# Kernel optimization log

Hardware: AMD Instinct MI355X
Metric: run time of the kernel (lower is better)

## Reference

```python
import jax, jax.numpy as jnp
import numpy as np
import math

B, T, C = 2, 1024, 1024
H = 16
HS = C // H          # head size 64
ROT = HS // 2        # rotary dims 32
TT = 1024            # ctx_len
FFN = 4 * C
EPS = 1e-6


def _layernorm(x, g, b):
    m = jnp.mean(x, -1, keepdims=True)
    v = jnp.mean((x - m) ** 2, -1, keepdims=True)
    return (x - m) * jax.lax.rsqrt(v + EPS) * g + b


def _time_shift_half(x):
    # ZeroPad2d((0,0,1,-1)) applied to first half of channels: shift by one step in time
    c = x.shape[-1]
    a = jnp.pad(x[:, :, : c // 2], ((0, 0), (1, 0), (0, 0)))[:, :-1, :]
    return jnp.concatenate([a, x[:, :, c // 2 :]], axis=-1)


def _rotate_half(x):
    x1, x2 = jnp.split(x, 2, axis=-1)
    return jnp.concatenate([-x2, x1], axis=-1)


def _rotary_cos_sin(t_len, rot, base):
    inv_freq = 1.0 / (base ** (jnp.arange(0, rot, 2, dtype=jnp.float32) / rot))
    freqs = jnp.arange(t_len, dtype=jnp.float32)[:, None] * inv_freq[None, :]
    emb = jnp.concatenate([freqs, freqs], axis=-1)  # (T, rot)
    return jnp.cos(emb), jnp.sin(emb)


def _build_w(time_w, time_alpha, time_beta, t_len):
    # faithful translation of the pad/tile/reshape circulant trick
    w = jnp.pad(time_w, ((0, 0), (0, TT)))            # (H, 2TT)
    w = jnp.tile(w, (1, TT))                          # (H, 2TT*TT)
    w = w[:, :-TT].reshape(-1, TT, 2 * TT - 1)        # (H, TT, 2TT-1)
    w = w[:, :, TT - 1 :]                             # (H, TT, TT)
    return w[:, :t_len, :t_len] * time_alpha[:, :, :t_len] * time_beta[:, :t_len, :]


def setup_inputs() -> dict:
    key = jax.random.key(0)
    ks = jax.random.split(key, 24)
    s = 0.02
    d = {
        "x": jax.random.normal(ks[0], (B, T, C), jnp.float32),
        "ln1_g": jnp.ones((C,), jnp.float32),
        "ln1_b": jnp.zeros((C,), jnp.float32),
        "Wq": jax.random.normal(ks[1], (C, C), jnp.float32) * s,
        "bq": jnp.zeros((C,), jnp.float32),
        "Wk": jax.random.normal(ks[2], (C, C), jnp.float32) * s,
        "bk": jnp.zeros((C,), jnp.float32),
        "Wv": jax.random.normal(ks[3], (C, C), jnp.float32) * s,
        "bv": jnp.zeros((C,), jnp.float32),
        "Wo": jax.random.normal(ks[4], (C, C), jnp.float32) * s,
        "bo": jnp.zeros((C,), jnp.float32),
        "time_w": 1.0 + 0.01 * jax.random.normal(ks[5], (H, TT), jnp.float32),
        "time_alpha": 1.0 + 0.01 * jax.random.normal(ks[6], (H, 1, TT), jnp.float32),
        "time_beta": 1.0 + 0.01 * jax.random.normal(ks[7], (H, TT, 1), jnp.float32),
        "time_gamma": 1.0 + 0.01 * jax.random.normal(ks[8], (TT, 1), jnp.float32),
        "Wmix": jnp.eye(H, dtype=jnp.float32) + 0.01 * jax.random.normal(ks[9], (H, H), jnp.float32),
        "ln2_g": jnp.ones((C,), jnp.float32),
        "ln2_b": jnp.zeros((C,), jnp.float32),
        "Wgk": jax.random.normal(ks[10], (C, FFN), jnp.float32) * s,
        "bgk": jnp.zeros((FFN,), jnp.float32),
        "Wgv": jax.random.normal(ks[11], (C, FFN), jnp.float32) * s,
        "bgv": jnp.zeros((FFN,), jnp.float32),
        "Wgw": jax.random.normal(ks[12], (FFN, C), jnp.float32) * s,
        "bgw": jnp.zeros((C,), jnp.float32),
    }
    return d


def _block(x, ln1_g, ln1_b, Wq, bq, Wk, bk, Wv, bv, Wo, bo,
           time_w, time_alpha, time_beta, time_gamma, Wmix,
           ln2_g, ln2_b, Wgk, bgk, Wgv, bgv, Wgw, bgw):
    b, t, c = x.shape
    # ---- MHA_pro attention sublayer (pre-LN residual) ----
    xs = _time_shift_half(_layernorm(x, ln1_g, ln1_b))
    q = (xs @ Wq + bq).reshape(b, t, H, HS).transpose(0, 2, 1, 3)  # bhtd
    k = (xs @ Wk + bk).reshape(b, t, H, HS).transpose(0, 2, 1, 3)
    v = (xs @ Wv + bv).reshape(b, t, H, HS).transpose(0, 2, 1, 3)
    qr, qp = q[..., :ROT], q[..., ROT:]
    kr, kp = k[..., :ROT], k[..., ROT:]
    cos, sin = _rotary_cos_sin(t, ROT, float(TT))  # base = ctx_len
    qr = qr * cos + _rotate_half(qr) * sin
    kr = kr * cos + _rotate_half(kr) * sin
    q = jnp.concatenate([qr, qp], axis=-1)
    k = jnp.concatenate([kr, kp], axis=-1)
    att = jnp.einsum("bhtd,bhud->bhtu", q, k) * (1.0 / math.sqrt(HS))
    causal = jnp.tril(jnp.ones((t, t), bool))
    att = jnp.where(causal, att, -jnp.inf)
    att = jax.nn.softmax(att, axis=-1)
    w = _build_w(time_w, time_alpha, time_beta, t)  # (H, T, T)
    att = att * w[None]
    att = jnp.einsum("ij,bjtu->bitu", Wmix, att)  # 1x1 conv head mix
    y = jnp.einsum("bhtu,bhud->bhtd", att, v)
    y = y.transpose(0, 2, 1, 3).reshape(b, t, c)
    y = (y @ Wo + bo) * time_gamma[:t, :]
    x = x + y
    # ---- GeGLU MLP sublayer (pre-LN residual) ----
    xm = _layernorm(x, ln2_g, ln2_b)
    kk = xm @ Wgk + bgk
    vv = xm @ Wgv + bgv
    y2 = (jax.nn.gelu(kk, approximate=False) * vv) @ Wgw + bgw
    return x + y2


def reference(x, ln1_g, ln1_b, Wq, bq, Wk, bk, Wv, bv, Wo, bo,
              time_w, time_alpha, time_beta, time_gamma, Wmix,
              ln2_g, ln2_b, Wgk, bgk, Wgv, bgv, Wgw, bgw):
    return _block(x, ln1_g, ln1_b, Wq, bq, Wk, bk, Wv, bv, Wo, bo,
                  time_w, time_alpha, time_beta, time_gamma, Wmix,
                  ln2_g, ln2_b, Wgk, bgk, Wgv, bgv, Wgw, bgw)
```

## Files before the change

kernel.cpp:

```cpp
#include <hip/hip_runtime.h>
#include <math.h>

typedef unsigned short u16;
typedef short s16x8 __attribute__((ext_vector_type(8)));
typedef float f32x4 __attribute__((ext_vector_type(4)));

#define TB 2
#define TSEQ 1024
#define CC 1024
#define NH 16
#define HSZ 64
#define FFN 4096
#define MROWS (TB*TSEQ)

#define GLOAD16(g, l) __builtin_amdgcn_global_load_lds( \
    (const __attribute__((address_space(1))) unsigned*)(g), \
    (__attribute__((address_space(3))) unsigned*)(l), 16, 0, 0)

#define SBAR()  __builtin_amdgcn_s_barrier()
#define SCHED0() __builtin_amdgcn_sched_barrier(0)
#define LGKM0() asm volatile("s_waitcnt lgkmcnt(0)" ::: "memory")
#define WAITV4() asm volatile("s_waitcnt vmcnt(4)" ::: "memory")
#define PRIO(n) __builtin_amdgcn_s_setprio(n)

__device__ __forceinline__ float bf2f(u16 u){
  union { unsigned u; float f; } c; c.u = ((unsigned)u) << 16; return c.f;
}
__device__ __forceinline__ u16 f2bf(float f){
  union { float f; unsigned u; } c; c.f = f;
  unsigned u = c.u;
  u += 0x7fffu + ((u >> 16) & 1);
  return (u16)(u >> 16);
}
__device__ __forceinline__ float ldin(const void* p, size_t i, int bf){
  return bf ? bf2f(((const u16*)p)[i]) : ((const float*)p)[i];
}

__global__ void k_flag(const unsigned* __restrict__ g, int* __restrict__ flag){
  if (threadIdx.x == 0) *flag = (g[0] == 0x3F800000u) ? 0 : 1;
}

__global__ void k_transpose_cvt(const void* __restrict__ in, u16* __restrict__ out,
                                int R, int Cc, const int* __restrict__ flagp){
  int bf = *flagp;
  __shared__ u16 tile[32][33];
  int bx = blockIdx.x * 32, by = blockIdx.y * 32;
  int tx = threadIdx.x & 31, ty = threadIdx.x >> 5;
  #pragma unroll
  for (int i = 0; i < 32; i += 8)
    tile[ty + i][tx] = f2bf(ldin(in, (size_t)(by + ty + i) * Cc + bx + tx, bf));
  __syncthreads();
  #pragma unroll
  for (int i = 0; i < 32; i += 8)
    out[(size_t)(bx + ty + i) * R + by + tx] = tile[tx][ty + i];
}

__global__ void k_cvt(const void* __restrict__ in, u16* __restrict__ out, int n,
                      const int* __restrict__ flagp){
  int bf = *flagp;
  int i = blockIdx.x * 256 + threadIdx.x;
  if (i < n) out[i] = f2bf(ldin(in, i, bf));
}

__global__ void k_tw8(const void* __restrict__ tw, u16* __restrict__ tw8,
                      const int* __restrict__ flagp){
  int bf = *flagp;
  int idx = blockIdx.x*256 + threadIdx.x;
  int s = idx >> 14;
  int h = (idx >> 10) & 15;
  int k = idx & 1023;
  float v = (k + s < 1024) ? ldin(tw, h*1024 + k + s, bf) : 0.f;
  tw8[idx] = f2bf(v);
}

__global__ void k_ln1_shift(const void* __restrict__ x, const void* __restrict__ g,
                            const void* __restrict__ bta, u16* __restrict__ xs,
                            const int* __restrict__ flagp){
  int bf = *flagp;
  int row = blockIdx.x;
  int t = row & (TSEQ - 1);
  int tid = threadIdx.x;
  float v[4]; float s = 0.f, ss = 0.f;
  #pragma unroll
  for (int i = 0; i < 4; i++){
    v[i] = ldin(x, (size_t)row * CC + tid*4 + i, bf);
    s += v[i]; ss += v[i]*v[i];
  }
  __shared__ float rs[256], rss[256];
  rs[tid] = s; rss[tid] = ss; __syncthreads();
  for (int o = 128; o > 0; o >>= 1){ if (tid < o){ rs[tid] += rs[tid+o]; rss[tid] += rss[tid+o]; } __syncthreads(); }
  float mean = rs[0] * (1.0f/CC);
  float var  = rss[0] * (1.0f/CC) - mean*mean;
  float inv  = rsqrtf(var + 1e-6f);
  #pragma unroll
  for (int i = 0; i < 4; i++){
    int c = tid*4 + i;
    float o = (v[i]-mean)*inv*ldin(g, c, bf) + ldin(bta, c, bf);
    u16 ob = f2bf(o);
    if (c >= CC/2)            xs[(size_t)row*CC + c] = ob;
    else if (t < TSEQ-1)      xs[(size_t)(row+1)*CC + c] = ob;
  }
  if (t == 0 && tid < 128){
    #pragma unroll
    for (int i = 0; i < 4; i++) xs[(size_t)row*CC + tid*4 + i] = 0;
  }
}

__global__ void k_ln2(const float* __restrict__ x1, const void* __restrict__ g,
                      const void* __restrict__ bta, u16* __restrict__ xm,
                      const int* __restrict__ flagp){
  int bf = *flagp;
  int row = blockIdx.x;
  int tid = threadIdx.x;
  const float* xr = x1 + (size_t)row * CC;
  float v[4]; float s = 0.f, ss = 0.f;
  #pragma unroll
  for (int i = 0; i < 4; i++){ v[i] = xr[tid*4 + i]; s += v[i]; ss += v[i]*v[i]; }
  __shared__ float rs[256], rss[256];
  rs[tid] = s; rss[tid] = ss; __syncthreads();
  for (int o = 128; o > 0; o >>= 1){ if (tid < o){ rs[tid] += rs[tid+o]; rss[tid] += rss[tid+o]; } __syncthreads(); }
  float mean = rs[0] * (1.0f/CC);
  float var  = rss[0] * (1.0f/CC) - mean*mean;
  float inv  = rsqrtf(var + 1e-6f);
  #pragma unroll
  for (int i = 0; i < 4; i++){
    int c = tid*4 + i;
    xm[(size_t)row*CC + c] = f2bf((v[i]-mean)*inv*ldin(g, c, bf) + ldin(bta, c, bf));
  }
}

__global__ void k_rotary(u16* __restrict__ qkv){
  int idx = blockIdx.x*256 + threadIdx.x;
  int i = idx & 15;
  int h = (idx >> 4) & (NH-1);
  int row = idx >> 8;
  int t = row & (TSEQ-1);
  float invf = exp2f(-0.625f * (float)i);
  float ang = (float)t * invf;
  float cs = cosf(ang), sn = sinf(ang);
  size_t base = (size_t)row * (3*CC);
  u16* qp = qkv + base + h*HSZ;
  float a = bf2f(qp[i]), b2 = bf2f(qp[i+16]);
  qp[i]    = f2bf(a*cs - b2*sn);
  qp[i+16] = f2bf(b2*cs + a*sn);
  u16* kp = qkv + base + CC + h*HSZ;
  a = bf2f(kp[i]); b2 = bf2f(kp[i+16]);
  kp[i]    = f2bf(a*cs - b2*sn);
  kp[i+16] = f2bf(b2*cs + a*sn);
}

__global__ __launch_bounds__(256) void k_qk(
    const u16* __restrict__ qkv, u16* __restrict__ att)
{
  int m0 = blockIdx.y * 128;
  int n0 = blockIdx.x * 128;
  if (n0 > m0) return;
  int bh = blockIdx.z; int b = bh >> 4, h = bh & 15;
  __shared__ u16 As[128*32];
  __shared__ u16 Bs[128*32];
  int tid = threadIdx.x;
  int w = tid >> 6;
  int lane = tid & 63;
  int wm = (w >> 1) * 64, wn = (w & 1) * 64;
  f32x4 acc[4][4];
  #pragma unroll
  for (int i = 0; i < 4; i++)
    #pragma unroll
    for (int j = 0; j < 4; j++) acc[i][j] = (f32x4){0.f,0.f,0.f,0.f};

  int rr = lane >> 2;
  int cc = lane & 3;
  const u16* gA0 = qkv + (size_t)(b*TSEQ + m0 + w*32 + rr)*(3*CC) + h*HSZ + cc*8;
  const u16* gA1 = gA0 + (size_t)16*(3*CC);
  const u16* gB0 = qkv + (size_t)(b*TSEQ + n0 + w*32 + rr)*(3*CC) + CC + h*HSZ + cc*8;
  const u16* gB1 = gB0 + (size_t)16*(3*CC);
  u16* lA0 = As + (w*32)*32;
  u16* lA1 = As + (w*32+16)*32;
  u16* lB0 = Bs + (w*32)*32;
  u16* lB1 = Bs + (w*32+16)*32;
  int quad = lane >> 4;
  int l15 = lane & 15;

  #pragma unroll
  for (int k0 = 0; k0 < HSZ; k0 += 32){
    __syncthreads();
    GLOAD16(gA0 + k0, lA0);
    GLOAD16(gA1 + k0, lA1);
    GLOAD16(gB0 + k0, lB0);
    GLOAD16(gB1 + k0, lB1);
    __syncthreads();
    s16x8 af[4], bfr[4];
    #pragma unroll
    for (int i = 0; i < 4; i++){
      af[i]  = *(s16x8*)&As[(wm + i*16 + l15)*32 + quad*8];
      bfr[i] = *(s16x8*)&Bs[(wn + i*16 + l15)*32 + quad*8];
    }
    #pragma unroll
    for (int mi = 0; mi < 4; mi++)
      #pragma unroll
      for (int ni = 0; ni < 4; ni++)
        acc[mi][ni] = __builtin_amdgcn_mfma_f32_16x16x32_bf16(af[mi], bfr[ni], acc[mi][ni], 0, 0, 0);
  }

  #pragma unroll
  for (int mi = 0; mi < 4; mi++){
    int rowb = m0 + wm + mi*16 + quad*4;
    #pragma unroll
    for (int ni = 0; ni < 4; ni++){
      int col = n0 + wn + ni*16 + l15;
      #pragma unroll
      for (int r = 0; r < 4; r++){
        int t = rowb + r;
        att[((size_t)bh*TSEQ + t)*TSEQ + col] = f2bf(acc[mi][ni][r] * 0.125f);
      }
    }
  }
}

__global__ __launch_bounds__(256) void k_softmix(
    u16* __restrict__ att, const u16* __restrict__ tw8, const u16* __restrict__ al16,
    const u16* __restrict__ be16, const void* __restrict__ wmix,
    const int* __restrict__ flagp)
{
  int bf = *flagp;
  int bt = blockIdx.x;
  int t = bt & (TSEQ-1);
  int b = bt >> 10;
  int tid = threadIdx.x;
  int wv = tid >> 6;
  int lane = tid & 63;
  int tile_end = ((t >> 7) + 1) << 7;
  int nchunk = (t >> 9) + 1;
  int sh = (TSEQ-1 - t) & 7;
  int base = (TSEQ-1 - t) - sh;
  __shared__ __align__(16) u16 P[NH][TSEQ];
  __shared__ float wm[NH*NH];
  if (tid < NH*NH) wm[tid] = ldin(wmix, tid, bf);

  #pragma unroll
  for (int hi = 0; hi < 4; hi++){
    int h = wv*4 + hi;
    const u16* srow = att + ((size_t)(b*NH + h)*TSEQ + t)*TSEQ;
    const u16* twp  = tw8 + ((size_t)sh*NH + h)*TSEQ + base;
    const u16* alp  = al16 + h*TSEQ;
    float v[16];
    float lmax = -1e30f;
    for (int r = 0; r < nchunk; r++){
      int ub = lane*8 + r*512;
      uint4 pk = *(const uint4*)(srow + ub);
      const u16* pe = (const u16*)&pk;
      #pragma unroll
      for (int e = 0; e < 8; e++){
        float s = bf2f(pe[e]);
        if (ub + e > t) s = -1e30f;
        v[r*8+e] = s;
        lmax = fmaxf(lmax, s);
      }
    }
    #pragma unroll
    for (int o = 32; o > 0; o >>= 1) lmax = fmaxf(lmax, __shfl_xor(lmax, o));
    float lsum = 0.f;
    for (int r = 0; r < nchunk; r++){
      #pragma unroll
      for (int e = 0; e < 8; e++){
        float p = __expf(v[r*8+e] - lmax);
        v[r*8+e] = p; lsum += p;
      }
    }
    #pragma unroll
    for (int o = 32; o > 0; o >>= 1) lsum += __shfl_xor(lsum, o);
    float btv = bf2f(be16[h*TSEQ + t]);
    float inv = btv / lsum;
    for (int r = 0; r < nchunk; r++){
      int ub = lane*8 + r*512;
      uint4 wk = *(const uint4*)(twp + ub);
      uint4 ak = *(const uint4*)(alp + ub);
      const u16* we = (const u16*)&wk;
      const u16* ae = (const u16*)&ak;
      u16 tmp[8];
      #pragma unroll
      for (int e = 0; e < 8; e++){
        float p = v[r*8+e] * inv * bf2f(we[e]) * bf2f(ae[e]);
        tmp[e] = f2bf(p);
      }
      *(uint4*)&P[h][ub] = *(uint4*)tmp;
    }
  }
  __syncthreads();

  int u0 = tid * 4;
  if (u0 < tile_end){
    #pragma unroll
    for (int half2 = 0; half2 < 2; half2++){
      float acc[8][4];
      #pragma unroll
      for (int i = 0; i < 8; i++)
        #pragma unroll
        for (int k = 0; k < 4; k++) acc[i][k] = 0.f;
      #pragma unroll
      for (int j = 0; j < 16; j++){
        uint2 pk = *(const uint2*)&P[j][u0];
        float p0 = bf2f((u16)(pk.x & 0xffff)), p1 = bf2f((u16)(pk.x >> 16));
        float p2 = bf2f((u16)(pk.y & 0xffff)), p3 = bf2f((u16)(pk.y >> 16));
        #pragma unroll
        for (int i2 = 0; i2 < 8; i2++){
          float w = wm[(half2*8 + i2)*NH + j];
          acc[i2][0] += w*p0; acc[i2][1] += w*p1; acc[i2][2] += w*p2; acc[i2][3] += w*p3;
        }
      }
      #pragma unroll
      for (int i2 = 0; i2 < 8; i2++){
        int i = half2*8 + i2;
        u16 tmp[4] = {f2bf(acc[i2][0]), f2bf(acc[i2][1]), f2bf(acc[i2][2]), f2bf(acc[i2][3])};
        *(uint2*)(att + ((size_t)(b*NH + i)*TSEQ + t)*TSEQ + u0) = *(uint2*)tmp;
      }
    }
  }
}

__global__ void k_vt(const u16* __restrict__ qkv, u16* __restrict__ vt){
  __shared__ u16 tile[32][33];
  int bh = blockIdx.z; int b = bh >> 4, h = bh & 15;
  int u0 = blockIdx.x * 32, d0 = blockIdx.y * 32;
  int tx = threadIdx.x & 31, ty = threadIdx.x >> 5;
  #pragma unroll
  for (int i = 0; i < 32; i += 8)
    tile[ty + i][tx] = qkv[(size_t)(b*TSEQ + u0 + ty + i)*(3*CC) + 2*CC + h*HSZ + d0 + tx];
  __syncthreads();
  #pragma unroll
  for (int i = 0; i < 32; i += 8)
    vt[((size_t)bh*HSZ + d0 + ty + i)*TSEQ + u0 + tx] = tile[tx][ty + i];
}

__global__ void k_gelumul(const u16* __restrict__ kkvv, u16* __restrict__ hh){
  int idx = blockIdx.x*256 + threadIdx.x;
  int m = idx >> 9;
  int j = (idx & 511) * 8;
  uint4 kk4 = *(const uint4*)(kkvv + (size_t)m*(2*FFN) + j);
  uint4 vv4 = *(const uint4*)(kkvv + (size_t)m*(2*FFN) + FFN + j);
  const u16* ks = (const u16*)&kk4;
  const u16* vs = (const u16*)&vv4;
  u16 out[8];
  #pragma unroll
  for (int e = 0; e < 8; e++){
    float kk = bf2f(ks[e]), vv = bf2f(vs[e]);
    float ge = 0.5f*kk*(1.0f + erff(kk*0.70710678f));
    out[e] = f2bf(ge*vv);
  }
  *(uint4*)(hh + (size_t)m*FFN + j) = *(uint4*)out;
}

__global__ __launch_bounds__(512, 2) void k_gemm256(
    const u16* __restrict__ A, const u16* __restrict__ Bt,
    const u16* __restrict__ bias, int M, int N, int K, int mode,
    u16* __restrict__ outp, float* __restrict__ partial)
{
  __shared__ u16 S[65536];
  u16* SA0 = S;
  u16* SB0 = S + 16384;
  u16* SA1 = S + 32768;
  u16* SB1 = S + 49152;

  int nwg = (int)(gridDim.x * gridDim.y * gridDim.z);
  int lin = (int)(blockIdx.x + gridDim.x * (blockIdx.y + gridDim.y * blockIdx.z));
  int nl  = (nwg & 7) ? lin : ((lin & 7) * (nwg >> 3) + (lin >> 3));
  int bx  = nl % (int)gridDim.x;
  int tq  = nl / (int)gridDim.x;
  int by  = tq % (int)gridDim.y;
  int bz  = tq / (int)gridDim.y;

  int m0 = by * 256, n0 = bx * 256;
  int kper = K / (int)gridDim.z;
  int kbeg = bz * kper;
  int nt = kper >> 6;
  int niter = nt >> 1;

  int tid = threadIdx.x;
  int w = tid >> 6, lane = tid & 63;
  int wm = w >> 2, wn = w & 3;
  int quad = lane >> 4, l15 = lane & 15;
  int l3 = lane >> 3, ch = (lane & 7) ^ l3;

  const u16* gA = A  + (size_t)(m0 + w*16 + l3) * K + ch*8 + kbeg;
  const u16* gB = Bt + (size_t)(n0 + w*16 + l3) * K + ch*8 + kbeg;
  const size_t hstep = (size_t)128 * K;
  const size_t rstep = (size_t)8 * K;

  int pc0 = quad ^ (l15 & 7);
  int pc1 = (4 + quad) ^ (l15 & 7);
  int aoff0 = (wm*128 + l15)*64 + pc0*8;
  int aoff1 = (wm*128 + l15)*64 + pc1*8;
  int boff0 = (wn*64 + l15)*64 + pc0*8;
  int boff1 = (wn*64 + l15)*64 + pc1*8;

  f32x4 acc[8][4];
  #pragma unroll
  for (int i = 0; i < 8; i++)
    #pragma unroll
    for (int j = 0; j < 4; j++) acc[i][j] = (f32x4){0.f,0.f,0.f,0.f};

  #define STG(gbase, sbase, h, ko) do{ \
      const u16* _g = (gbase) + (size_t)(h)*hstep + (ko); \
      u16* _l = (sbase) + ((h)*128 + w*16)*64; \
      GLOAD16(_g, _l); \
      GLOAD16(_g + rstep, _l + 512); \
    }while(0)

  #define LD_A(buf, MQ) do{ _Pragma("unroll") for (int _m = 0; _m < 4; _m++){ \
      a0[_m] = *(const s16x8*)((buf) + aoff0 + (MQ)*4096 + _m*1024); \
      a1[_m] = *(const s16x8*)((buf) + aoff1 + (MQ)*4096 + _m*1024); } }while(0)

  #define LD_B(buf, NQ, B0A, B1A) do{ _Pragma("unroll") for (int _n = 0; _n < 2; _n++){ \
      B0A[_n] = *(const s16x8*)((buf) + boff0 + (NQ)*2048 + _n*1024); \
      B1A[_n] = *(const s16x8*)((buf) + boff1 + (NQ)*2048 + _n*1024); } }while(0)

  #define MMQ(MQ, NQ, B0A, B1A) do{ _Pragma("unroll") for (int _m = 0; _m < 4; _m++){ \
      _Pragma("unroll") for (int _n = 0; _n < 2; _n++){ \
        acc[(MQ)*4+_m][(NQ)*2+_n] = __builtin_amdgcn_mfma_f32_16x16x32_bf16(a0[_m], B0A[_n], acc[(MQ)*4+_m][(NQ)*2+_n], 0, 0, 0); \
        acc[(MQ)*4+_m][(NQ)*2+_n] = __builtin_amdgcn_mfma_f32_16x16x32_bf16(a1[_m], B1A[_n], acc[(MQ)*4+_m][(NQ)*2+_n], 0, 0, 0); }} }while(0)

  STG(gB, SB0, 0, 0); STG(gB, SB0, 1, 0);
  STG(gA, SA0, 0, 0); STG(gA, SA0, 1, 0);
  STG(gB, SB1, 0, 64); STG(gB, SB1, 1, 64);
  WAITV4();
  SBAR();

  s16x8 a0[4], a1[4], bl0[2], bl1[2], bh0[2], bh1[2];

  for (int i = 0; i < niter; i++){
    int t1k = (2*i+1)*64;
    int t2k = (2*i+2 < nt) ? (2*i+2)*64 : 0;
    int t3k = (2*i+3 < nt) ? (2*i+3)*64 : 0;

    LD_A(SA0, 0); LD_B(SB0, 0, bl0, bl1);
    STG(gA, SA1, 0, t1k);
    SBAR(); LGKM0(); SCHED0(); PRIO(1); MMQ(0,0,bl0,bl1); PRIO(0); SBAR();
    LD_B(SB0, 1, bh0, bh1);
    STG(gA, SA1, 1, t1k);
    SBAR(); LGKM0(); SCHED0(); PRIO(1); MMQ(0,1,bh0,bh1); PRIO(0); SBAR();
    LD_A(SA0, 1);
    STG(gB, SB0, 0, t2k);
    SBAR(); LGKM0(); SCHED0(); PRIO(1); MMQ(1,0,bl0,bl1); PRIO(0); SBAR();
    STG(gB, SB0, 1, t2k);
    SBAR(); LGKM0(); SCHED0(); PRIO(1); MMQ(1,1,bh0,bh1); PRIO(0);
    WAITV4(); SBAR();
    LD_A(SA1, 0); LD_B(SB1, 0, bl0, bl1);
    STG(gA, SA0, 0, t2k);
    SBAR(); LGKM0(); SCHED0(); PRIO(1); MMQ(0,0,bl0,bl1); PRIO(0); SBAR();
    LD_B(SB1, 1, bh0, bh1);
    STG(gA, SA0, 1, t2k);
    SBAR(); LGKM0(); SCHED0(); PRIO(1); MMQ(0,1,bh0,bh1); PRIO(0); SBAR();
    LD_A(SA1, 1);
    STG(gB, SB1, 0, t3k);
    SBAR(); LGKM0(); SCHED0(); PRIO(1); MMQ(1,0,bl0,bl1); PRIO(0); SBAR();
    STG(gB, SB1, 1, t3k);
    SBAR(); LGKM0(); SCHED0(); PRIO(1); MMQ(1,1,bh0,bh1); PRIO(0);
    WAITV4(); SBAR();
  }

  if (mode == 3){
    float* pout = partial + (size_t)bz * M * N;
    #pragma unroll
    for (int mi = 0; mi < 8; mi++){
      int rowb = m0 + wm*128 + mi*16 + quad*4;
      #pragma unroll
      for (int ni = 0; ni < 4; ni++){
        int col = n0 + wn*64 + ni*16 + l15;
        #pragma unroll
        for (int r = 0; r < 4; r++)
          pout[(size_t)(rowb + r) * N + col] = acc[mi][ni][r];
      }
    }
  } else {
    #pragma unroll
    for (int mi = 0; mi < 8; mi++){
      int rowb = m0 + wm*128 + mi*16 + quad*4;
      #pragma unroll
      for (int ni = 0; ni < 4; ni++){
        int col = n0 + wn*64 + ni*16 + l15;
        float bv = bf2f(bias[col]);
        #pragma unroll
        for (int r = 0; r < 4; r++)
          outp[(size_t)(rowb + r) * N + col] = f2bf(acc[mi][ni][r] + bv);
      }
    }
  }
  #undef STG
  #undef LD_A
  #undef LD_B
  #undef MMQ
}

__global__ __launch_bounds__(256) void k_gemm(
    const u16* __restrict__ A, const u16* __restrict__ Bt,
    const u16* __restrict__ bias, int M, int N, int K, int mode,
    void* __restrict__ outp, const void* __restrict__ xres,
    const float* __restrict__ resf, const u16* __restrict__ gamma,
    float* __restrict__ partial, const int* __restrict__ flagp)
{
  int bf = *flagp;
  __shared__ u16 As[128*32];
  __shared__ u16 Bs[128*32];
  int tid = threadIdx.x;
  int m0 = blockIdx.y * 128;
  int n0 = blockIdx.x * 128;
  int nz = gridDim.z;
  int kper = K / nz;
  int kbeg = blockIdx.z * kper;
  int kend = kbeg + kper;
  int w = tid >> 6;
  int lane = tid & 63;
  int wm = (w >> 1) * 64, wn = (w & 1) * 64;
  f32x4 acc[4][4];
  #pragma unroll
  for (int i = 0; i < 4; i++)
    #pragma unroll
    for (int j = 0; j < 4; j++) acc[i][j] = (f32x4){0.f,0.f,0.f,0.f};

  int rr = lane >> 2;
  int cc = lane & 3;
  const u16* gA0 = A  + (size_t)(m0 + w*32 + rr)*K + cc*8;
  const u16* gA1 = gA0 + (size_t)16*K;
  const u16* gB0 = Bt + (size_t)(n0 + w*32 + rr)*K + cc*8;
  const u16* gB1 = gB0 + (size_t)16*K;
  u16* lA0 = As + (w*32)*32;
  u16* lA1 = As + (w*32+16)*32;
  u16* lB0 = Bs + (w*32)*32;
  u16* lB1 = Bs + (w*32+16)*32;
  int quad = lane >> 4;
  int l15 = lane & 15;

  for (int k0 = kbeg; k0 < kend; k0 += 32){
    __syncthreads();
    GLOAD16(gA0 + k0, lA0);
    GLOAD16(gA1 + k0, lA1);
    GLOAD16(gB0 + k0, lB0);
    GLOAD16(gB1 + k0, lB1);
    __syncthreads();
    s16x8 af[4], bfr[4];
    #pragma unroll
    for (int i = 0; i < 4; i++){
      af[i]  = *(s16x8*)&As[(wm + i*16 + l15)*32 + quad*8];
      bfr[i] = *(s16x8*)&Bs[(wn + i*16 + l15)*32 + quad*8];
    }
    #pragma unroll
    for (int mi = 0; mi < 4; mi++)
      #pragma unroll
      for (int ni = 0; ni < 4; ni++)
        acc[mi][ni] = __builtin_amdgcn_mfma_f32_16x16x32_bf16(af[mi], bfr[ni], acc[mi][ni], 0, 0, 0);
  }

  if (nz > 1){
    float* pout = partial + (size_t)blockIdx.z * M * N;
    #pragma unroll
    for (int mi = 0; mi < 4; mi++){
      int rowb = m0 + wm + mi*16 + quad*4;
      #pragma unroll
      for (int ni = 0; ni < 4; ni++){
        int col = n0 + wn + ni*16 + l15;
        #pragma unroll
        for (int r = 0; r < 4; r++)
          pout[(size_t)(rowb + r) * N + col] = acc[mi][ni][r];
      }
    }
    return;
  }

  #pragma unroll
  for (int mi = 0; mi < 4; mi++){
    int rowb = m0 + wm + mi*16 + quad*4;
    #pragma unroll
    for (int ni = 0; ni < 4; ni++){
      int col = n0 + wn + ni*16 + l15;
      float bv = bf2f(bias[col]);
      #pragma unroll
      for (int r = 0; r < 4; r++){
        int row = rowb + r;
        float val = acc[mi][ni][r] + bv;
        size_t idx = (size_t)row * N + col;
        if (mode == 0){
          ((u16*)outp)[idx] = f2bf(val);
        } else if (mode == 1){
          int t = row & (TSEQ-1);
          ((float*)outp)[idx] = ldin(xres, idx, bf) + val * bf2f(gamma[t]);
        } else {
          float o = resf[idx] + val;
          if (bf) ((u16*)outp)[idx] = f2bf(o);
          else    ((float*)outp)[idx] = o;
        }
      }
    }
  }
}

__global__ void k_reduceK(const float* __restrict__ partial, int nsplit,
                          int M, int N, const u16* __restrict__ bias, int mode,
                          void* __restrict__ outp, const void* __restrict__ xres,
                          const float* __restrict__ resf, const u16* __restrict__ gamma,
                          const int* __restrict__ flagp){
  int bf = *flagp;
  int idx = blockIdx.x*256 + threadIdx.x;
  int row = idx / (N/4);
  int c0  = (idx % (N/4)) * 4;
  size_t base = (size_t)row * N + c0;
  float v[4] = {0.f, 0.f, 0.f, 0.f};
  for (int s = 0; s < nsplit; s++){
    const float4 p = *(const float4*)(partial + (size_t)s * M * N + base);
    v[0] += p.x; v[1] += p.y; v[2] += p.z; v[3] += p.w;
  }
  #pragma unroll
  for (int e = 0; e < 4; e++) v[e] += bf2f(bias[c0 + e]);
  if (mode == 1){
    int t = row & (TSEQ-1);
    float gm = bf2f(gamma[t]);
    float o[4];
    #pragma unroll
    for (int e = 0; e < 4; e++) o[e] = ldin(xres, base + e, bf) + v[e] * gm;
    *(float4*)((float*)outp + base) = (float4){o[0], o[1], o[2], o[3]};
  } else {
    float o[4];
    #pragma unroll
    for (int e = 0; e < 4; e++) o[e] = resf[base + e] + v[e];
    if (bf){
      u16 tmp[4] = {f2bf(o[0]), f2bf(o[1]), f2bf(o[2]), f2bf(o[3])};
      *(uint2*)((u16*)outp + base) = *(uint2*)tmp;
    } else {
      *(float4*)((float*)outp + base) = (float4){o[0], o[1], o[2], o[3]};
    }
  }
}

__global__ __launch_bounds__(256) void k_pv(
    const u16* __restrict__ att, const u16* __restrict__ vt, u16* __restrict__ y)
{
  __shared__ u16 As[128*32];
  __shared__ u16 Bs[64*32];
  int tid = threadIdx.x;
  int bh = blockIdx.y; int b = bh >> 4, h = bh & 15;
  int m0 = blockIdx.x * 128;
  const u16* A  = att + (size_t)bh * TSEQ * TSEQ;
  const u16* Bt = vt  + (size_t)bh * HSZ * TSEQ;
  int w = tid >> 6;
  int lane = tid & 63;
  int wm = (w >> 1) * 64, wn = (w & 1) * 32;
  f32x4 acc[4][2];
  #pragma unroll
  for (int i = 0; i < 4; i++){ acc[i][0] = (f32x4){0,0,0,0}; acc[i][1] = (f32x4){0,0,0,0}; }

  int rr = lane >> 2;
  int cc = lane & 3;
  const u16* gA0 = A + (size_t)(m0 + w*32 + rr)*TSEQ + cc*8;
  const u16* gA1 = gA0 + (size_t)16*TSEQ;
  const u16* gB0 = Bt + (size_t)(w*16 + rr)*TSEQ + cc*8;
  u16* lA0 = As + (w*32)*32;
  u16* lA1 = As + (w*32+16)*32;
  u16* lB0 = Bs + (w*16)*32;
  int quad = lane >> 4;
  int l15 = lane & 15;
  int kend = m0 + 128;

  for (int k0 = 0; k0 < kend; k0 += 32){
    __syncthreads();
    GLOAD16(gA0 + k0, lA0);
    GLOAD16(gA1 + k0, lA1);
    GLOAD16(gB0 + k0, lB0);
    __syncthreads();
    s16x8 af[4], bfr[2];
    #pragma unroll
    for (int i = 0; i < 4; i++)
      af[i] = *(s16x8*)&As[(wm + i*16 + l15)*32 + quad*8];
    #pragma unroll
    for (int i = 0; i < 2; i++)
      bfr[i] = *(s16x8*)&Bs[(wn + i*16 + l15)*32 + quad*8];
    #pragma unroll
    for (int mi = 0; mi < 4; mi++)
      #pragma unroll
      for (int ni = 0; ni < 2; ni++)
        acc[mi][ni] = __builtin_amdgcn_mfma_f32_16x16x32_bf16(af[mi], bfr[ni], acc[mi][ni], 0, 0, 0);
  }

  #pragma unroll
  for (int mi = 0; mi < 4; mi++){
    int rowb = m0 + wm + mi*16 + quad*4;
    #pragma unroll
    for (int ni = 0; ni < 2; ni++){
      int col = wn + ni*16 + l15;
      #pragma unroll
      for (int r = 0; r < 4; r++){
        int t = rowb + r;
        y[(size_t)(b*TSEQ + t)*CC + h*HSZ + col] = f2bf(acc[mi][ni][r]);
      }
    }
  }
}

extern "C" void kernel_launch(void* const* d_in, const int* in_sizes, int n_in,
                              void* d_out, int out_size, void* d_ws, size_t ws_size,
                              hipStream_t stream){
  const void* x     = d_in[0];
  const void* ln1g  = d_in[1];
  const void* ln1b  = d_in[2];
  const void* Wq    = d_in[3];
  const void* bq    = d_in[4];
  const void* Wk    = d_in[5];
  const void* bk    = d_in[6];
  const void* Wv    = d_in[7];
  const void* bv    = d_in[8];
  const void* Wo    = d_in[9];
  const void* bo    = d_in[10];
  const void* timew = d_in[11];
  const void* alpha = d_in[12];
  const void* beta  = d_in[13];
  const void* gamma = d_in[14];
  const void* Wmix  = d_in[15];
  const void* ln2g  = d_in[16];
  const void* ln2b  = d_in[17];
  const void* Wgk   = d_in[18];
  const void* bgk   = d_in[19];
  const void* Wgv   = d_in[20];
  const void* bgv   = d_in[21];
  const void* Wgw   = d_in[22];
  const void* bgw   = d_in[23];

  char* ws = (char*)d_ws;
  size_t off = 0;
  auto carve = [&](size_t bytes)->char*{
    char* p = ws + off; off = (off + bytes + 255) & ~(size_t)255; return p;
  };
  int*  FLAG   = (int*)carve(256);
  u16*  WT_QKV = (u16*)carve(3072ull*1024*2);
  u16*  WT_O   = (u16*)carve(1024ull*1024*2);
  u16*  WT_G   = (u16*)carve(8192ull*1024*2);
  u16*  WT_W   = (u16*)carve(1024ull*4096*2);
  u16*  B_QKV  = (u16*)carve(3072*2);
  u16*  B_G    = (u16*)carve(8192*2);
  u16*  B_O    = (u16*)carve(1024*2);
  u16*  B_W    = (u16*)carve(1024*2);
  u16*  GMA    = (u16*)carve(1024*2);
  u16*  TW8    = (u16*)carve(8ull*16*1024*2 + 4096);
  u16*  AL16   = (u16*)carve(16*1024*2);
  u16*  BE16   = (u16*)carve(16*1024*2);
  u16*  XS     = (u16*)carve((size_t)MROWS*CC*2);
  u16*  QKV    = (u16*)carve((size_t)MROWS*3*CC*2);
  u16*  ATT    = (u16*)carve((size_t)TB*NH*TSEQ*TSEQ*2);
  u16*  VT     = (u16*)carve((size_t)TB*NH*HSZ*TSEQ*2);
  u16*  Y      = (u16*)carve((size_t)MROWS*CC*2);
  float* X1    = (float*)carve((size_t)MROWS*CC*4);
  u16*  XM     = (u16*)carve((size_t)MROWS*CC*2);
  u16*  KKVV   = (u16*)carve((size_t)MROWS*2*FFN*2);
  u16*  HH     = (u16*)carve((size_t)MROWS*FFN*2);
  float* PART  = (float*)ATT;
  (void)ws_size; (void)in_sizes; (void)n_in; (void)out_size;

  k_flag<<<1,64,0,stream>>>((const unsigned*)ln1g, FLAG);

  k_transpose_cvt<<<dim3(32,32),256,0,stream>>>(Wq, WT_QKV,                1024, 1024, FLAG);
  k_transpose_cvt<<<dim3(32,32),256,0,stream>>>(Wk, WT_QKV + 1024*1024,    1024, 1024, FLAG);
  k_transpose_cvt<<<dim3(32,32),256,0,stream>>>(Wv, WT_QKV + 2*1024*1024,  1024, 1024, FLAG);
  k_transpose_cvt<<<dim3(32,32),256,0,stream>>>(Wo, WT_O,                  1024, 1024, FLAG);
  k_transpose_cvt<<<dim3(128,32),256,0,stream>>>(Wgk, WT_G,                1024, 4096, FLAG);
  k_transpose_cvt<<<dim3(128,32),256,0,stream>>>(Wgv, WT_G + 4096ull*1024, 1024, 4096, FLAG);
  k_transpose_cvt<<<dim3(32,128),256,0,stream>>>(Wgw, WT_W,                4096, 1024, FLAG);
  k_cvt<<<4,256,0,stream>>>(bq, B_QKV,        1024, FLAG);
  k_cvt<<<4,256,0,stream>>>(bk, B_QKV + 1024, 1024, FLAG);
  k_cvt<<<4,256,0,stream>>>(bv, B_QKV + 2048, 1024, FLAG);
  k_cvt<<<16,256,0,stream>>>(bgk, B_G,        4096, FLAG);
  k_cvt<<<16,256,0,stream>>>(bgv, B_G + 4096, 4096, FLAG);
  k_cvt<<<4,256,0,stream>>>(bo,  B_O, 1024, FLAG);
  k_cvt<<<4,256,0,stream>>>(bgw, B_W, 1024, FLAG);
  k_cvt<<<4,256,0,stream>>>(gamma, GMA, 1024, FLAG);
  k_tw8<<<512,256,0,stream>>>(timew, TW8, FLAG);
  k_cvt<<<64,256,0,stream>>>(alpha, AL16, 16384, FLAG);
  k_cvt<<<64,256,0,stream>>>(beta,  BE16, 16384, FLAG);

  k_ln1_shift<<<MROWS,256,0,stream>>>(x, ln1g, ln1b, XS, FLAG);
  k_gemm256<<<dim3(12,8),512,0,stream>>>(XS, WT_QKV, B_QKV, MROWS, 3072, 1024, 0,
                                         QKV, nullptr);
  k_rotary<<<2048,256,0,stream>>>(QKV);
  k_qk<<<dim3(8,8,TB*NH),256,0,stream>>>(QKV, ATT);
  k_softmix<<<TB*TSEQ,256,0,stream>>>(ATT, TW8, AL16, BE16, Wmix, FLAG);
  k_vt<<<dim3(32,2,32),256,0,stream>>>(QKV, VT);
  k_pv<<<dim3(8,32),256,0,stream>>>(ATT, VT, Y);

  k_gemm<<<dim3(8,16,2),256,0,stream>>>(Y, WT_O, B_O, MROWS, 1024, 1024, 1,
                                        nullptr, nullptr, nullptr, nullptr, PART, FLAG);
  k_reduceK<<<MROWS*1024/(4*256),256,0,stream>>>(PART, 2, MROWS, 1024, B_O, 1,
                                                 X1, x, nullptr, GMA, FLAG);

  k_ln2<<<MROWS,256,0,stream>>>(X1, ln2g, ln2b, XM, FLAG);
  k_gemm256<<<dim3(32,8),512,0,stream>>>(XM, WT_G, B_G, MROWS, 8192, 1024, 0,
                                         KKVV, nullptr);
  k_gelumul<<<(MROWS*FFN)/(256*8),256,0,stream>>>(KKVV, HH);

  k_gemm256<<<dim3(4,8,8),512,0,stream>>>(HH, WT_W, nullptr, MROWS, 1024, 4096, 3,
                                          nullptr, PART);
  k_reduceK<<<MROWS*1024/(4*256),256,0,stream>>>(PART, 8, MROWS, 1024, B_W, 2,
                                                 d_out, nullptr, X1, nullptr, FLAG);
}
```

Before: 440.8 us.

## Warp-shuffle layernorm reductions, rope table, and restructured softmix loads/mixing

Replaces the shared-memory tree reductions in both layernorm kernels with wavefront shuffles plus a four-entry cross-wave sum. Precomputes the rotary cos/sin table once so the rotary kernel no longer evaluates transcendentals. In the softmax/head-mix kernel, all score rows are loaded up front together with the time-weight and alpha vectors, the chunk loops are unrolled explicitly, and the 16x16 head mix is restructured so each thread covers two columns for all heads and loops only over the causal extent. The intent is less launch, reduction and memory-latency overhead, at the cost of more registers in softmix, which now has an occupancy hint.

```diff
diff --git a/kernel.cpp b/kernel.cpp
--- a/kernel.cpp
+++ b/kernel.cpp
@@ -73,6 +73,15 @@
   tw8[idx] = f2bf(v);
 }
 
+__global__ void k_ropetab(float2* __restrict__ rt){
+  int idx = blockIdx.x*256 + threadIdx.x;
+  int i = idx & 15;
+  int t = idx >> 4;
+  float invf = exp2f(-0.625f * (float)i);
+  float ang = (float)t * invf;
+  rt[idx] = (float2){cosf(ang), sinf(ang)};
+}
+
 __global__ void k_ln1_shift(const void* __restrict__ x, const void* __restrict__ g,
                             const void* __restrict__ bta, u16* __restrict__ xs,
                             const int* __restrict__ flagp){
@@ -80,17 +89,22 @@
   int row = blockIdx.x;
   int t = row & (TSEQ - 1);
   int tid = threadIdx.x;
+  int wv = tid >> 6, lane = tid & 63;
   float v[4]; float s = 0.f, ss = 0.f;
   #pragma unroll
   for (int i = 0; i < 4; i++){
     v[i] = ldin(x, (size_t)row * CC + tid*4 + i, bf);
     s += v[i]; ss += v[i]*v[i];
   }
-  __shared__ float rs[256], rss[256];
-  rs[tid] = s; rss[tid] = ss; __syncthreads();
-  for (int o = 128; o > 0; o >>= 1){ if (tid < o){ rs[tid] += rs[tid+o]; rss[tid] += rss[tid+o]; } __syncthreads(); }
-  float mean = rs[0] * (1.0f/CC);
-  float var  = rss[0] * (1.0f/CC) - mean*mean;
+  #pragma unroll
+  for (int o = 32; o > 0; o >>= 1){ s += __shfl_xor(s, o); ss += __shfl_xor(ss, o); }
+  __shared__ float rs[4], rss[4];
+  if (lane == 0){ rs[wv] = s; rss[wv] = ss; }
+  __syncthreads();
+  float S = rs[0]+rs[1]+rs[2]+rs[3];
+  float SS = rss[0]+rss[1]+rss[2]+rss[3];
+  float mean = S * (1.0f/CC);
+  float var  = SS * (1.0f/CC) - mean*mean;
   float inv  = rsqrtf(var + 1e-6f);
   #pragma unroll
   for (int i = 0; i < 4; i++){
@@ -112,15 +126,20 @@
   int bf = *flagp;
   int row = blockIdx.x;
   int tid = threadIdx.x;
+  int wv = tid >> 6, lane = tid & 63;
   const float* xr = x1 + (size_t)row * CC;
   float v[4]; float s = 0.f, ss = 0.f;
   #pragma unroll
   for (int i = 0; i < 4; i++){ v[i] = xr[tid*4 + i]; s += v[i]; ss += v[i]*v[i]; }
-  __shared__ float rs[256], rss[256];
-  rs[tid] = s; rss[tid] = ss; __syncthreads();
-  for (int o = 128; o > 0; o >>= 1){ if (tid < o){ rs[tid] += rs[tid+o]; rss[tid] += rss[tid+o]; } __syncthreads(); }
-  float mean = rs[0] * (1.0f/CC);
-  float var  = rss[0] * (1.0f/CC) - mean*mean;
+  #pragma unroll
+  for (int o = 32; o > 0; o >>= 1){ s += __shfl_xor(s, o); ss += __shfl_xor(ss, o); }
+  __shared__ float rs[4], rss[4];
+  if (lane == 0){ rs[wv] = s; rss[wv] = ss; }
+  __syncthreads();
+  float S = rs[0]+rs[1]+rs[2]+rs[3];
+  float SS = rss[0]+rss[1]+rss[2]+rss[3];
+  float mean = S * (1.0f/CC);
+  float var  = SS * (1.0f/CC) - mean*mean;
   float inv  = rsqrtf(var + 1e-6f);
   #pragma unroll
   for (int i = 0; i < 4; i++){
@@ -129,15 +148,14 @@
   }
 }
 
-__global__ void k_rotary(u16* __restrict__ qkv){
+__global__ void k_rotary(u16* __restrict__ qkv, const float2* __restrict__ rt){
   int idx = blockIdx.x*256 + threadIdx.x;
   int i = idx & 15;
   int h = (idx >> 4) & (NH-1);
   int row = idx >> 8;
   int t = row & (TSEQ-1);
-  float invf = exp2f(-0.625f * (float)i);
-  float ang = (float)t * invf;
-  float cs = cosf(ang), sn = sinf(ang);
+  float2 cssn = rt[t*16 + i];
+  float cs = cssn.x, sn = cssn.y;
   size_t base = (size_t)row * (3*CC);
   u16* qp = qkv + base + h*HSZ;
   float a = bf2f(qp[i]), b2 = bf2f(qp[i+16]);
@@ -217,7 +235,7 @@
   }
 }
 
-__global__ __launch_bounds__(256) void k_softmix(
+__global__ __launch_bounds__(256, 4) void k_softmix(
     u16* __restrict__ att, const u16* __restrict__ tw8, const u16* __restrict__ al16,
     const u16* __restrict__ be16, const void* __restrict__ wmix,
     const int* __restrict__ flagp)
@@ -237,83 +255,98 @@
   __shared__ float wm[NH*NH];
   if (tid < NH*NH) wm[tid] = ldin(wmix, tid, bf);
 
+  uint4 raw[4][2];
+  #pragma unroll
+  for (int hi = 0; hi < 4; hi++){
+    const u16* srow = att + ((size_t)(b*NH + wv*4 + hi)*TSEQ + t)*TSEQ + lane*8;
+    raw[hi][0] = *(const uint4*)srow;
+    if (nchunk == 2) raw[hi][1] = *(const uint4*)(srow + 512);
+  }
+
   #pragma unroll
   for (int hi = 0; hi < 4; hi++){
     int h = wv*4 + hi;
-    const u16* srow = att + ((size_t)(b*NH + h)*TSEQ + t)*TSEQ;
-    const u16* twp  = tw8 + ((size_t)sh*NH + h)*TSEQ + base;
-    const u16* alp  = al16 + h*TSEQ;
-    float v[16];
+    const u16* twp = tw8 + ((size_t)sh*NH + h)*TSEQ + base + lane*8;
+    const u16* alp = al16 + h*TSEQ + lane*8;
+    uint4 wk2[2], ak2[2];
+    wk2[0] = *(const uint4*)twp;
+    ak2[0] = *(const uint4*)alp;
+    if (nchunk == 2){
+      wk2[1] = *(const uint4*)(twp + 512);
+      ak2[1] = *(const uint4*)(alp + 512);
+    }
+
+    float v0[8], v1[8];
     float lmax = -1e30f;
-    for (int r = 0; r < nchunk; r++){
-      int ub = lane*8 + r*512;
-      uint4 pk = *(const uint4*)(srow + ub);
-      const u16* pe = (const u16*)&pk;
+    {
+      const u16* pe = (const u16*)&raw[hi][0];
+      int ub = lane*8;
       #pragma unroll
       for (int e = 0; e < 8; e++){
-        float s = bf2f(pe[e]);
-        if (ub + e > t) s = -1e30f;
-        v[r*8+e] = s;
-        lmax = fmaxf(lmax, s);
+        float s2 = bf2f(pe[e]);
+        if (ub + e > t) s2 = -1e30f;
+        v0[e] = s2; lmax = fmaxf(lmax, s2);
+      }
+    }
+    if (nchunk == 2){
+      const u16* pe = (const u16*)&raw[hi][1];
+      int ub = lane*8 + 512;
+      #pragma unroll
+      for (int e = 0; e < 8; e++){
+        float s2 = bf2f(pe[e]);
+        if (ub + e > t) s2 = -1e30f;
+        v1[e] = s2; lmax = fmaxf(lmax, s2);
       }
     }
     #pragma unroll
     for (int o = 32; o > 0; o >>= 1) lmax = fmaxf(lmax, __shfl_xor(lmax, o));
     float lsum = 0.f;
-    for (int r = 0; r < nchunk; r++){
-      #pragma unroll
-      for (int e = 0; e < 8; e++){
-        float p = __expf(v[r*8+e] - lmax);
-        v[r*8+e] = p; lsum += p;
+    #pragma unroll
+    for (int e = 0; e < 8; e++){ float p = __expf(v0[e]-lmax); v0[e] = p; lsum += p; }
+    if (nchunk == 2){
+      #pragma unroll
+      for (int e = 0; e < 8; e++){ float p = __expf(v1[e]-lmax); v1[e] = p; lsum += p; }
+    }
+    #pragma unroll
+    for (int o = 32; o > 0; o >>= 1) lsum += __shfl_xor(lsum, o);
+    float inv = bf2f(be16[h*TSEQ + t]) / lsum;
+    {
+      const u16* we = (const u16*)&wk2[0];
+      const u16* ae = (const u16*)&ak2[0];
+      u16 tmp[8];
+      #pragma unroll
+      for (int e = 0; e < 8; e++) tmp[e] = f2bf(v0[e]*inv*bf2f(we[e])*bf2f(ae[e]));
+      *(uint4*)&P[h][lane*8] = *(uint4*)tmp;
+    }
+    if (nchunk == 2){
+      const u16* we = (const u16*)&wk2[1];
+      const u16* ae = (const u16*)&ak2[1];
+      u16 tmp[8];
+      #pragma unroll
+      for (int e = 0; e < 8; e++) tmp[e] = f2bf(v1[e]*inv*bf2f(we[e])*bf2f(ae[e]));
+      *(uint4*)&P[h][lane*8+512] = *(uint4*)tmp;
+    }
+  }
+  __syncthreads();
+
+  for (int u0 = tid*2; u0 < tile_end; u0 += 512){
+    float acc[16][2];
+    #pragma unroll
+    for (int i = 0; i < 16; i++){ acc[i][0] = 0.f; acc[i][1] = 0.f; }
+    #pragma unroll
+    for (int j = 0; j < 16; j++){
+      unsigned pk = *(const unsigned*)&P[j][u0];
+      float p0 = bf2f((u16)(pk & 0xffff)), p1 = bf2f((u16)(pk >> 16));
+      #pragma unroll
+      for (int i = 0; i < 16; i++){
+        float w = wm[i*NH + j];
+        acc[i][0] += w*p0; acc[i][1] += w*p1;
       }
     }
     #pragma unroll
-    for (int o = 32; o > 0; o >>= 1) lsum += __shfl_xor(lsum, o);
-    float btv = bf2f(be16[h*TSEQ + t]);
-    float inv = btv / lsum;
-    for (int r = 0; r < nchunk; r++){
-      int ub = lane*8 + r*512;
-      uint4 wk = *(const uint4*)(twp + ub);
-      uint4 ak = *(const uint4*)(alp + ub);
-      const u16* we = (const u16*)&wk;
-      const u16* ae = (const u16*)&ak;
-      u16 tmp[8];
-      #pragma unroll
-      for (int e = 0; e < 8; e++){
-        float p = v[r*8+e] * inv * bf2f(we[e]) * bf2f(ae[e]);
-        tmp[e] = f2bf(p);
-      }
-      *(uint4*)&P[h][ub] = *(uint4*)tmp;
-    }
-  }
-  __syncthreads();
-
-  int u0 = tid * 4;
-  if (u0 < tile_end){
-    #pragma unroll
-    for (int half2 = 0; half2 < 2; half2++){
-      float acc[8][4];
-      #pragma unroll
-      for (int i = 0; i < 8; i++)
-        #pragma unroll
-        for (int k = 0; k < 4; k++) acc[i][k] = 0.f;
-      #pragma unroll
-      for (int j = 0; j < 16; j++){
-        uint2 pk = *(const uint2*)&P[j][u0];
-        float p0 = bf2f((u16)(pk.x & 0xffff)), p1 = bf2f((u16)(pk.x >> 16));
-        float p2 = bf2f((u16)(pk.y & 0xffff)), p3 = bf2f((u16)(pk.y >> 16));
-        #pragma unroll
-        for (int i2 = 0; i2 < 8; i2++){
-          float w = wm[(half2*8 + i2)*NH + j];
-          acc[i2][0] += w*p0; acc[i2][1] += w*p1; acc[i2][2] += w*p2; acc[i2][3] += w*p3;
-        }
-      }
-      #pragma unroll
-      for (int i2 = 0; i2 < 8; i2++){
-        int i = half2*8 + i2;
-        u16 tmp[4] = {f2bf(acc[i2][0]), f2bf(acc[i2][1]), f2bf(acc[i2][2]), f2bf(acc[i2][3])};
-        *(uint2*)(att + ((size_t)(b*NH + i)*TSEQ + t)*TSEQ + u0) = *(uint2*)tmp;
-      }
+    for (int i = 0; i < 16; i++){
+      u16 tmp[2] = {f2bf(acc[i][0]), f2bf(acc[i][1])};
+      *(unsigned*)(att + ((size_t)(b*NH + i)*TSEQ + t)*TSEQ + u0) = *(unsigned*)tmp;
     }
   }
 }
@@ -749,10 +782,12 @@
   u16*  XM     = (u16*)carve((size_t)MROWS*CC*2);
   u16*  KKVV   = (u16*)carve((size_t)MROWS*2*FFN*2);
   u16*  HH     = (u16*)carve((size_t)MROWS*FFN*2);
+  float2* RT   = (float2*)carve((size_t)TSEQ*16*8);
   float* PART  = (float*)ATT;
   (void)ws_size; (void)in_sizes; (void)n_in; (void)out_size;
 
   k_flag<<<1,64,0,stream>>>((const unsigned*)ln1g, FLAG);
+  k_ropetab<<<64,256,0,stream>>>(RT);
 
   k_transpose_cvt<<<dim3(32,32),256,0,stream>>>(Wq, WT_QKV,                1024, 1024, FLAG);
   k_transpose_cvt<<<dim3(32,32),256,0,stream>>>(Wk, WT_QKV + 1024*1024,    1024, 1024, FLAG);
@@ -776,7 +811,7 @@
   k_ln1_shift<<<MROWS,256,0,stream>>>(x, ln1g, ln1b, XS, FLAG);
   k_gemm256<<<dim3(12,8),512,0,stream>>>(XS, WT_QKV, B_QKV, MROWS, 3072, 1024, 0,
                                          QKV, nullptr);
-  k_rotary<<<2048,256,0,stream>>>(QKV);
+  k_rotary<<<2048,256,0,stream>>>(QKV, RT);
   k_qk<<<dim3(8,8,TB*NH),256,0,stream>>>(QKV, ATT);
   k_softmix<<<TB*TSEQ,256,0,stream>>>(ATT, TW8, AL16, BE16, Wmix, FLAG);
   k_vt<<<dim3(32,2,32),256,0,stream>>>(QKV, VT);
```

After: 618.6 us. +40.3%, slower.
